# Kernel optimization log

Measured on AMD Instinct MI355X. Metric: run time of the kernel, lower is better.

The kernel has to match this reference:

```python
import jax, jax.numpy as jnp
import numpy as np

S = 512       # number of rnn_output rows (source positions)
T = 512       # number of target rows (queries)
DU = 512      # dim_u
DT = 512      # dim_target
D = DU + DT   # concat dim


def setup_inputs() -> dict:
    key = jax.random.key(0)
    k1, k2, k3, k4, k5, k6 = jax.random.split(key, 6)
    return {
        "rnn_outputs": jax.random.normal(k1, (S, DU), dtype=jnp.float32),
        "target": jax.random.normal(k2, (T, DT), dtype=jnp.float32),
        # nn.Linear(D, D): weight [D, D], bias [D]
        "W_lin": jax.random.normal(k3, (D, D), dtype=jnp.float32) * 0.02,
        "b_lin": jax.random.normal(k4, (D,), dtype=jnp.float32) * 0.02,
        # nn.Linear(D, 1): weight [1, D] stored flat, bias scalar
        "w_score": jax.random.normal(k5, (D,), dtype=jnp.float32) * 0.02,
        "b_score": jax.random.normal(k6, (), dtype=jnp.float32) * 0.02,
    }


def reference(rnn_outputs, target, W_lin, b_lin, w_score, b_score):
    du = rnn_outputs.shape[1]
    # linear(concat([rnn, tgt])) == rnn @ W[:, :du].T + tgt @ W[:, du:].T + b
    # (split the weight instead of materializing the [T, S, D] concat)
    A = rnn_outputs @ W_lin[:, :du].T            # [S, D]
    B = target @ W_lin[:, du:].T + b_lin         # [T, D]
    h = jnp.tanh(B[:, None, :] + A[None, :, :])  # [T, S, D]
    scores = h @ w_score + b_score               # [T, S]
    weights = jax.nn.softmax(scores, axis=1)     # softmax over source dim S
    # stack of per-row weighted sums == weights @ rnn_outputs
    return weights @ rnn_outputs                 # [T, dim_u]
```

## Files before the change

kernel.cpp:

```cpp
#include <hip/hip_runtime.h>


#define C2F 2.8853900817779268f

typedef __attribute__((ext_vector_type(8))) short short8;
typedef __attribute__((ext_vector_type(4))) float f32x4;
typedef __attribute__((ext_vector_type(2))) float f32x2;

__device__ __forceinline__ unsigned short bf16_rne(float f) {
    unsigned u = __builtin_bit_cast(unsigned, f);
    unsigned r = (u + 0x7FFFu + ((u >> 16) & 1u)) >> 16;
    return (unsigned short)r;
}
__device__ __forceinline__ float bf16_f(unsigned short h) {
    unsigned u = ((unsigned)h) << 16;
    return __builtin_bit_cast(float, u);
}
__device__ __forceinline__ f32x2 splat2(float s) {
    f32x2 r; r.x = s; r.y = s; return r;
}

__global__ __launch_bounds__(256, 4) void k1_mfma(
    const float* __restrict__ rnn, const float* __restrict__ tgt,
    const float* __restrict__ W, const float* __restrict__ bl,
    float* __restrict__ Abuf, float* __restrict__ Bbuf, int ksplit)
{
    __shared__ unsigned short Xh[64][40], Xl[64][40], Wh[64][40], Wl[64][40];
    const int j0 = blockIdx.x * 64;
    const int i0 = blockIdx.y * 64;
    const int kz = blockIdx.z;
    const int klen = 512 / ksplit;
    const int kbase = kz * klen;
    const bool isB = (i0 >= 512);
    const float* __restrict__ X = isB ? tgt : rnn;
    const int irow0 = isB ? (i0 - 512) : i0;
    const int koff = isB ? 512 : 0;
    const int tid = threadIdx.x;
    const int lane = tid & 63;
    const int wv = tid >> 6;
    const int isub = (wv & 1) * 32;
    const int jsub = (wv >> 1) * 32;
    const int srow = tid >> 2;
    const int skq  = tid & 3;
    const float* __restrict__ xp = X + (size_t)(irow0 + srow) * 512 + kbase + skq * 8;
    const float* __restrict__ wp = W + (size_t)(j0 + srow) * 1024 + koff + kbase + skq * 8;
    const int frow = lane & 15;
    const int fk   = (lane >> 4) * 8;
    f32x4 acc00 = {0.f,0.f,0.f,0.f}, acc01 = {0.f,0.f,0.f,0.f};
    f32x4 acc10 = {0.f,0.f,0.f,0.f}, acc11 = {0.f,0.f,0.f,0.f};
    float4 xv0 = *(const float4*)(xp);
    float4 xv1 = *(const float4*)(xp + 4);
    float4 wv0 = *(const float4*)(wp);
    float4 wv1 = *(const float4*)(wp + 4);
    for (int k0 = 0; k0 < klen; k0 += 32) {
        __syncthreads();
        {
            short8 xh8, xl8, wh8, wl8;
            const float xf[8] = {xv0.x, xv0.y, xv0.z, xv0.w, xv1.x, xv1.y, xv1.z, xv1.w};
            const float wf[8] = {wv0.x, wv0.y, wv0.z, wv0.w, wv1.x, wv1.y, wv1.z, wv1.w};
            #pragma unroll
            for (int e = 0; e < 8; ++e) {
                const unsigned short xh = bf16_rne(xf[e]);
                const unsigned short wh = bf16_rne(wf[e]);
                xh8[e] = (short)xh;
                wh8[e] = (short)wh;
                xl8[e] = (short)bf16_rne(xf[e] - bf16_f(xh));
                wl8[e] = (short)bf16_rne(wf[e] - bf16_f(wh));
            }
            *(short8*)&Xh[srow][skq * 8] = xh8;
            *(short8*)&Xl[srow][skq * 8] = xl8;
            *(short8*)&Wh[srow][skq * 8] = wh8;
            *(short8*)&Wl[srow][skq * 8] = wl8;
        }
        __syncthreads();
        if (k0 + 32 < klen) {
            xv0 = *(const float4*)(xp + k0 + 32);
            xv1 = *(const float4*)(xp + k0 + 36);
            wv0 = *(const float4*)(wp + k0 + 32);
            wv1 = *(const float4*)(wp + k0 + 36);
        }
        const short8 ah0 = *(const short8*)&Xh[isub + frow][fk];
        const short8 ah1 = *(const short8*)&Xh[isub + 16 + frow][fk];
        const short8 bh0 = *(const short8*)&Wh[jsub + frow][fk];
        const short8 bh1 = *(const short8*)&Wh[jsub + 16 + frow][fk];
        acc00 = __builtin_amdgcn_mfma_f32_16x16x32_bf16(ah0, bh0, acc00, 0, 0, 0);
        acc01 = __builtin_amdgcn_mfma_f32_16x16x32_bf16(ah0, bh1, acc01, 0, 0, 0);
        acc10 = __builtin_amdgcn_mfma_f32_16x16x32_bf16(ah1, bh0, acc10, 0, 0, 0);
        acc11 = __builtin_amdgcn_mfma_f32_16x16x32_bf16(ah1, bh1, acc11, 0, 0, 0);
        const short8 al0 = *(const short8*)&Xl[isub + frow][fk];
        const short8 al1 = *(const short8*)&Xl[isub + 16 + frow][fk];
        acc00 = __builtin_amdgcn_mfma_f32_16x16x32_bf16(al0, bh0, acc00, 0, 0, 0);
        acc01 = __builtin_amdgcn_mfma_f32_16x16x32_bf16(al0, bh1, acc01, 0, 0, 0);
        acc10 = __builtin_amdgcn_mfma_f32_16x16x32_bf16(al1, bh0, acc10, 0, 0, 0);
        acc11 = __builtin_amdgcn_mfma_f32_16x16x32_bf16(al1, bh1, acc11, 0, 0, 0);
        const short8 bl0 = *(const short8*)&Wl[jsub + frow][fk];
        const short8 bl1 = *(const short8*)&Wl[jsub + 16 + frow][fk];
        acc00 = __builtin_amdgcn_mfma_f32_16x16x32_bf16(ah0, bl0, acc00, 0, 0, 0);
        acc01 = __builtin_amdgcn_mfma_f32_16x16x32_bf16(ah0, bl1, acc01, 0, 0, 0);
        acc10 = __builtin_amdgcn_mfma_f32_16x16x32_bf16(ah1, bl0, acc10, 0, 0, 0);
        acc11 = __builtin_amdgcn_mfma_f32_16x16x32_bf16(ah1, bl1, acc11, 0, 0, 0);
    }
    const int orow = (lane >> 4) * 4;
    const int ocol = lane & 15;
    float* __restrict__ dst = (isB ? Bbuf : Abuf) + (size_t)kz * 524288;
    const bool addb = isB && (kz == ksplit - 1);
#define K1ST(ACC, MT, NT) do {                                            \
    const int jl = jsub + (NT)*16 + ocol;                                 \
    const float bb = addb ? bl[j0 + jl] : 0.f;                            \
    const int il = isub + (MT)*16 + orow;                                 \
    float4 o;                                                             \
    o.x = (ACC[0] + bb) * C2F;                                            \
    o.y = (ACC[1] + bb) * C2F;                                            \
    o.z = (ACC[2] + bb) * C2F;                                            \
    o.w = (ACC[3] + bb) * C2F;                                            \
    *(float4*)(dst + (size_t)(j0 + jl) * 512 + irow0 + il) = o;           \
} while (0)
    K1ST(acc00, 0, 0); K1ST(acc01, 0, 1); K1ST(acc10, 1, 0); K1ST(acc11, 1, 1);
#undef K1ST
}

#define K2P(ACC, PP, RR) do {                                                  \
    const f32x2 e0_ = __builtin_elementwise_fma(A0.PP, splat2(B0.RR), one2);   \
    const f32x2 e1_ = __builtin_elementwise_fma(A1.PP, splat2(B1.RR), one2);   \
    const f32x2 e2_ = __builtin_elementwise_fma(A2.PP, splat2(B2.RR), one2);   \
    const f32x2 e3_ = __builtin_elementwise_fma(A3.PP, splat2(B3.RR), one2);   \
    const f32x2 l01_ = e0_ * e1_;                                              \
    const f32x2 l23_ = e2_ * e3_;                                              \
    const f32x2 n01_ = __builtin_elementwise_fma(wx2, e1_, wy2 * e0_);         \
    const f32x2 n23_ = __builtin_elementwise_fma(wz2, e3_, ww2 * e2_);         \
    const f32x2 N_   = __builtin_elementwise_fma(n01_, l23_, n23_ * l01_);     \
    const f32x2 D_   = l01_ * l23_;                                            \
    f32x2 rd_;                                                                 \
    rd_.x = __builtin_amdgcn_rcpf(D_.x);                                       \
    rd_.y = __builtin_amdgcn_rcpf(D_.y);                                       \
    ACC = __builtin_elementwise_fma(N_, rd_, ACC);                             \
} while (0)

#define K2EXP(P0, P1) __builtin_amdgcn_exp2f(__builtin_fmaf(sumf, (P1), (P0)))

__global__ __launch_bounds__(256, 4) void k2_scores(
    const float* __restrict__ A0T, const float* __restrict__ A1T,
    const float* __restrict__ B0T, const float* __restrict__ B1T,
    const float* __restrict__ wsc, float* __restrict__ P, int dchunk, float sumf)
{
    __shared__ float at[32][68];
    __shared__ float bt[32][68];
    __shared__ float wl[128];
    const int s0 = blockIdx.x * 64;
    const int t0 = blockIdx.y * 64;
    const int dz = blockIdx.z * dchunk;
    const int tid = threadIdx.x;
    if (tid < dchunk) wl[tid] = wsc[dz + tid];
    const int drow = tid >> 3;
    const int sc8  = (tid & 7) * 8;
    const int ti   = tid >> 4;
    const int tj   = tid & 15;
    const float* __restrict__ Ar0 = A0T + (size_t)(dz + drow) * 512 + s0 + sc8;
    const float* __restrict__ Ar1 = A1T + (size_t)(dz + drow) * 512 + s0 + sc8;
    const float* __restrict__ Br0 = B0T + (size_t)(dz + drow) * 512 + t0 + sc8;
    const float* __restrict__ Br1 = B1T + (size_t)(dz + drow) * 512 + t0 + sc8;
    const f32x2 one2 = splat2(1.f);
    f32x2 ac0l = splat2(0.f), ac0h = splat2(0.f);
    f32x2 ac1l = splat2(0.f), ac1h = splat2(0.f);
    f32x2 ac2l = splat2(0.f), ac2h = splat2(0.f);
    f32x2 ac3l = splat2(0.f), ac3h = splat2(0.f);
    float4 pa00 = *(const float4*)(Ar0);
    float4 pa01 = *(const float4*)(Ar0 + 4);
    float4 pa10 = *(const float4*)(Ar1);
    float4 pa11 = *(const float4*)(Ar1 + 4);
    float4 pb00 = *(const float4*)(Br0);
    float4 pb01 = *(const float4*)(Br0 + 4);
    float4 pb10 = *(const float4*)(Br1);
    float4 pb11 = *(const float4*)(Br1 + 4);
    for (int c0 = 0; c0 < dchunk; c0 += 32) {
        __syncthreads();
        {
            float4 ea0, ea1, eb0, eb1;
            ea0.x = K2EXP(pa00.x, pa10.x);
            ea0.y = K2EXP(pa00.y, pa10.y);
            ea0.z = K2EXP(pa00.z, pa10.z);
            ea0.w = K2EXP(pa00.w, pa10.w);
            ea1.x = K2EXP(pa01.x, pa11.x);
            ea1.y = K2EXP(pa01.y, pa11.y);
            ea1.z = K2EXP(pa01.z, pa11.z);
            ea1.w = K2EXP(pa01.w, pa11.w);
            eb0.x = K2EXP(pb00.x, pb10.x);
            eb0.y = K2EXP(pb00.y, pb10.y);
            eb0.z = K2EXP(pb00.z, pb10.z);
            eb0.w = K2EXP(pb00.w, pb10.w);
            eb1.x = K2EXP(pb01.x, pb11.x);
            eb1.y = K2EXP(pb01.y, pb11.y);
            eb1.z = K2EXP(pb01.z, pb11.z);
            eb1.w = K2EXP(pb01.w, pb11.w);
            *(float4*)&at[drow][sc8]     = ea0;
            *(float4*)&at[drow][sc8 + 4] = ea1;
            *(float4*)&bt[drow][sc8]     = eb0;
            *(float4*)&bt[drow][sc8 + 4] = eb1;
        }
        __syncthreads();
        if (c0 + 32 < dchunk) {
            const size_t off = (size_t)(c0 + 32) * 512;
            pa00 = *(const float4*)(Ar0 + off);
            pa01 = *(const float4*)(Ar0 + off + 4);
            pa10 = *(const float4*)(Ar1 + off);
            pa11 = *(const float4*)(Ar1 + off + 4);
            pb00 = *(const float4*)(Br0 + off);
            pb01 = *(const float4*)(Br0 + off + 4);
            pb10 = *(const float4*)(Br1 + off);
            pb11 = *(const float4*)(Br1 + off + 4);
        }
        for (int dd = 0; dd < 32; dd += 4) {
            const float4 wa = *(const float4*)&wl[c0 + dd];
            const f32x2 wx2 = splat2(wa.x);
            const f32x2 wy2 = splat2(wa.y);
            const f32x2 wz2 = splat2(wa.z);
            const f32x2 ww2 = splat2(wa.w);
            const f32x4 A0 = *(const f32x4*)&at[dd + 0][tj * 4];
            const f32x4 A1 = *(const f32x4*)&at[dd + 1][tj * 4];
            const f32x4 A2 = *(const f32x4*)&at[dd + 2][tj * 4];
            const f32x4 A3 = *(const f32x4*)&at[dd + 3][tj * 4];
            const f32x4 B0 = *(const f32x4*)&bt[dd + 0][ti * 4];
            const f32x4 B1 = *(const f32x4*)&bt[dd + 1][ti * 4];
            const f32x4 B2 = *(const f32x4*)&bt[dd + 2][ti * 4];
            const f32x4 B3 = *(const f32x4*)&bt[dd + 3][ti * 4];
            K2P(ac0l, xy, x); K2P(ac0h, zw, x);
            K2P(ac1l, xy, y); K2P(ac1h, zw, y);
            K2P(ac2l, xy, z); K2P(ac2h, zw, z);
            K2P(ac3l, xy, w); K2P(ac3h, zw, w);
        }
    }
    float* __restrict__ Pz = P + (size_t)blockIdx.z * 512 * 512;
    float4 o0, o1, o2, o3;
    o0.x = ac0l.x; o0.y = ac0l.y; o0.z = ac0h.x; o0.w = ac0h.y;
    o1.x = ac1l.x; o1.y = ac1l.y; o1.z = ac1h.x; o1.w = ac1h.y;
    o2.x = ac2l.x; o2.y = ac2l.y; o2.z = ac2h.x; o2.w = ac2h.y;
    o3.x = ac3l.x; o3.y = ac3l.y; o3.z = ac3h.x; o3.w = ac3h.y;
    *(float4*)(Pz + (size_t)(t0 + ti * 4 + 0) * 512 + s0 + tj * 4) = o0;
    *(float4*)(Pz + (size_t)(t0 + ti * 4 + 1) * 512 + s0 + tj * 4) = o1;
    *(float4*)(Pz + (size_t)(t0 + ti * 4 + 2) * 512 + s0 + tj * 4) = o2;
    *(float4*)(Pz + (size_t)(t0 + ti * 4 + 3) * 512 + s0 + tj * 4) = o3;
}

__global__ __launch_bounds__(256, 4) void k3_softmax(
    const float* __restrict__ P, float* __restrict__ wgt, int nz)
{
    __shared__ float wm[4];
    __shared__ float wsum[4];
    const int t = blockIdx.x;
    const int tid = threadIdx.x;
    const size_t base = (size_t)t * 512 + tid * 2;
    float sx = 0.f, sy = 0.f;
    for (int z = 0; z < nz; ++z) {
        const float2 p = *(const float2*)(P + base + (size_t)z * 262144);
        sx += p.x; sy += p.y;
    }
    const float x0 = -2.f * sx;
    const float x1 = -2.f * sy;
    float m = fmaxf(x0, x1);
    #pragma unroll
    for (int off = 32; off; off >>= 1) m = fmaxf(m, __shfl_xor(m, off));
    if ((tid & 63) == 0) wm[tid >> 6] = m;
    __syncthreads();
    m = fmaxf(fmaxf(wm[0], wm[1]), fmaxf(wm[2], wm[3]));
    const float L2E = 1.4426950408889634f;
    const float e0 = __builtin_amdgcn_exp2f((x0 - m) * L2E);
    const float e1 = __builtin_amdgcn_exp2f((x1 - m) * L2E);
    float s = e0 + e1;
    #pragma unroll
    for (int off = 32; off; off >>= 1) s += __shfl_xor(s, off);
    if ((tid & 63) == 0) wsum[tid >> 6] = s;
    __syncthreads();
    s = wsum[0] + wsum[1] + wsum[2] + wsum[3];
    const float inv = 1.0f / s;
    float2 o; o.x = e0 * inv; o.y = e1 * inv;
    *(float2*)(wgt + (size_t)t * 512 + tid * 2) = o;
}

#define K4BFRAG(BH, BL, DCOL) do {                                      \
    _Pragma("unroll")                                                   \
    for (int e = 0; e < 8; ++e) {                                       \
        const float v_ = rs[fk + e][(DCOL)];                            \
        const unsigned short h_ = bf16_rne(v_);                         \
        (BH)[e] = (short)h_;                                            \
        (BL)[e] = (short)bf16_rne(v_ - bf16_f(h_));                     \
    }                                                                   \
} while (0)

__global__ __launch_bounds__(256, 4) void k4_mfma(
    const float* __restrict__ wgt, const float* __restrict__ rnn,
    float* __restrict__ P4)
{
    __shared__ unsigned short Gh[64][40], Gl[64][40];
    __shared__ float rs[32][69];
    const int d0g = blockIdx.x * 64;
    const int t0g = blockIdx.y * 64;
    const int z   = blockIdx.z;
    const int tid = threadIdx.x;
    const int lane = tid & 63;
    const int wv = tid >> 6;
    const int tsub = (wv & 1) * 32;
    const int dsub = (wv >> 1) * 32;
    const int trow = tid >> 2, skq = tid & 3;
    const int srw  = tid >> 3, cq  = tid & 7;
    const int frow = lane & 15;
    const int fk   = (lane >> 4) * 8;
    const int sbase = z * 64;
    f32x4 acc00 = {0.f,0.f,0.f,0.f}, acc01 = {0.f,0.f,0.f,0.f};
    f32x4 acc10 = {0.f,0.f,0.f,0.f}, acc11 = {0.f,0.f,0.f,0.f};
    const float* __restrict__ gp = wgt + (size_t)(t0g + trow) * 512 + sbase + skq * 8;
    const float* __restrict__ rp = rnn + (size_t)(sbase + srw) * 512 + d0g + cq * 8;
    float4 g0 = *(const float4*)(gp);
    float4 g1 = *(const float4*)(gp + 4);
    float4 r0 = *(const float4*)(rp);
    float4 r1 = *(const float4*)(rp + 4);
    #pragma unroll
    for (int c = 0; c < 2; ++c) {
        __syncthreads();
        {
            short8 gh8, gl8;
            const float gf[8] = {g0.x,g0.y,g0.z,g0.w,g1.x,g1.y,g1.z,g1.w};
            #pragma unroll
            for (int e = 0; e < 8; ++e) {
                const unsigned short h = bf16_rne(gf[e]);
                gh8[e] = (short)h;
                gl8[e] = (short)bf16_rne(gf[e] - bf16_f(h));
            }
            *(short8*)&Gh[trow][skq * 8] = gh8;
            *(short8*)&Gl[trow][skq * 8] = gl8;
            *(float4*)&rs[srw][cq * 8]     = r0;
            *(float4*)&rs[srw][cq * 8 + 4] = r1;
        }
        __syncthreads();
        if (c == 0) {
            g0 = *(const float4*)(gp + 32);
            g1 = *(const float4*)(gp + 36);
            r0 = *(const float4*)(rp + 32 * 512);
            r1 = *(const float4*)(rp + 32 * 512 + 4);
        }
        const short8 ah0 = *(const short8*)&Gh[tsub + frow][fk];
        const short8 ah1 = *(const short8*)&Gh[tsub + 16 + frow][fk];
        const short8 al0 = *(const short8*)&Gl[tsub + frow][fk];
        const short8 al1 = *(const short8*)&Gl[tsub + 16 + frow][fk];
        short8 bh0, bl0, bh1, bl1;
        K4BFRAG(bh0, bl0, dsub + frow);
        K4BFRAG(bh1, bl1, dsub + 16 + frow);
        acc00 = __builtin_amdgcn_mfma_f32_16x16x32_bf16(ah0, bh0, acc00, 0, 0, 0);
        acc01 = __builtin_amdgcn_mfma_f32_16x16x32_bf16(ah0, bh1, acc01, 0, 0, 0);
        acc10 = __builtin_amdgcn_mfma_f32_16x16x32_bf16(ah1, bh0, acc10, 0, 0, 0);
        acc11 = __builtin_amdgcn_mfma_f32_16x16x32_bf16(ah1, bh1, acc11, 0, 0, 0);
        acc00 = __builtin_amdgcn_mfma_f32_16x16x32_bf16(al0, bh0, acc00, 0, 0, 0);
        acc01 = __builtin_amdgcn_mfma_f32_16x16x32_bf16(al0, bh1, acc01, 0, 0, 0);
        acc10 = __builtin_amdgcn_mfma_f32_16x16x32_bf16(al1, bh0, acc10, 0, 0, 0);
        acc11 = __builtin_amdgcn_mfma_f32_16x16x32_bf16(al1, bh1, acc11, 0, 0, 0);
        acc00 = __builtin_amdgcn_mfma_f32_16x16x32_bf16(ah0, bl0, acc00, 0, 0, 0);
        acc01 = __builtin_amdgcn_mfma_f32_16x16x32_bf16(ah0, bl1, acc01, 0, 0, 0);
        acc10 = __builtin_amdgcn_mfma_f32_16x16x32_bf16(ah1, bl0, acc10, 0, 0, 0);
        acc11 = __builtin_amdgcn_mfma_f32_16x16x32_bf16(ah1, bl1, acc11, 0, 0, 0);
    }
    const int orow = (lane >> 4) * 4;
    const int ocol = lane & 15;
    float* __restrict__ Pz = P4 + (size_t)z * 262144;
#define K4ST(ACC, MT, NT) do {                                           \
    const int tl = tsub + (MT)*16 + orow;                                \
    const int dl = dsub + (NT)*16 + ocol;                                \
    float* p = Pz + (size_t)(t0g + tl) * 512 + d0g + dl;                 \
    p[0]    = ACC[0];                                                    \
    p[512]  = ACC[1];                                                    \
    p[1024] = ACC[2];                                                    \
    p[1536] = ACC[3];                                                    \
} while (0)
    K4ST(acc00, 0, 0); K4ST(acc01, 0, 1); K4ST(acc10, 1, 0); K4ST(acc11, 1, 1);
#undef K4ST
}

__global__ __launch_bounds__(256, 4) void k5_reduce(
    const float* __restrict__ P4, float* __restrict__ out)
{
    const int i = (blockIdx.x * 256 + threadIdx.x) * 4;
    float4 a = *(const float4*)(P4 + i);
    #pragma unroll
    for (int z = 1; z < 8; ++z) {
        const float4 b = *(const float4*)(P4 + (size_t)z * 262144 + i);
        a.x += b.x; a.y += b.y; a.z += b.z; a.w += b.w;
    }
    *(float4*)(out + i) = a;
}

extern "C" void kernel_launch(void* const* d_in, const int* in_sizes, int n_in,
                              void* d_out, int out_size, void* d_ws, size_t ws_size,
                              hipStream_t stream) {
    const float* rnn = (const float*)d_in[0];
    const float* tgt = (const float*)d_in[1];
    const float* W   = (const float*)d_in[2];
    const float* bl  = (const float*)d_in[3];
    const float* wsc = (const float*)d_in[4];
    float* out = (float*)d_out;

    const int nz = 8;
    const int dchunk = 1024 / nz;
    float* ws = (float*)d_ws;

    const bool split = (ws_size >= 17825792u);

    if (split) {
        float* A   = ws;
        float* B   = ws + 2 * 524288;
        float* P   = ws + 4 * 524288;
        float* wgt = P + (size_t)nz * 262144;
        float* P4  = P;
        k1_mfma   <<<dim3(16, 16, 2), 256, 0, stream>>>(rnn, tgt, W, bl, A, B, 2);
        k2_scores <<<dim3(8, 8, nz),  256, 0, stream>>>(A, A + 524288, B, B + 524288,
                                                        wsc, P, dchunk, 1.f);
        k3_softmax<<<512,             256, 0, stream>>>(P, wgt, nz);
        k4_mfma   <<<dim3(8, 8, 8),   256, 0, stream>>>(wgt, rnn, P4);
        k5_reduce <<<256,             256, 0, stream>>>(P4, out);
    } else {
        float* A   = ws;
        float* B   = ws + 524288;
        float* P   = ws + 2 * 524288;
        float* wgt = P + (size_t)nz * 262144;
        float* P4  = P;
        k1_mfma   <<<dim3(16, 16, 1), 256, 0, stream>>>(rnn, tgt, W, bl, A, B, 1);
        k2_scores <<<dim3(8, 8, nz),  256, 0, stream>>>(A, A, B, B, wsc, P, dchunk, 0.f);
        k3_softmax<<<512,             256, 0, stream>>>(P, wgt, nz);
        k4_mfma   <<<dim3(8, 8, 8),   256, 0, stream>>>(wgt, rnn, P4);
        k5_reduce <<<256,             256, 0, stream>>>(P4, out);
    }
}
```

Baseline: 55.74 us.

## Double-buffer LDS tiles in score kernel to overlap exp/stores with compute

Splits the score kernel's shared tiles into two ping-pong buffers. The exp transform and LDS write of the next d-chunk now happen while the current chunk is being computed, so one barrier per chunk is removed. The loop is hardcoded to 4 chunks of 32, which assumes dchunk equals 128 and ignores the runtime dchunk argument. It also doubles LDS use per block, which may limit occupancy.

```diff
diff --git a/kernel.cpp b/kernel.cpp
--- a/kernel.cpp
+++ b/kernel.cpp
@@ -120,10 +120,10 @@
 }
 
 #define K2P(ACC, PP, RR) do {                                                  \
-    const f32x2 e0_ = __builtin_elementwise_fma(A0.PP, splat2(B0.RR), one2);   \
-    const f32x2 e1_ = __builtin_elementwise_fma(A1.PP, splat2(B1.RR), one2);   \
-    const f32x2 e2_ = __builtin_elementwise_fma(A2.PP, splat2(B2.RR), one2);   \
-    const f32x2 e3_ = __builtin_elementwise_fma(A3.PP, splat2(B3.RR), one2);   \
+    const f32x2 e0_ = __builtin_elementwise_fma(A_0.PP, splat2(B_0.RR), one2); \
+    const f32x2 e1_ = __builtin_elementwise_fma(A_1.PP, splat2(B_1.RR), one2); \
+    const f32x2 e2_ = __builtin_elementwise_fma(A_2.PP, splat2(B_2.RR), one2); \
+    const f32x2 e3_ = __builtin_elementwise_fma(A_3.PP, splat2(B_3.RR), one2); \
     const f32x2 l01_ = e0_ * e1_;                                              \
     const f32x2 l23_ = e2_ * e3_;                                              \
     const f32x2 n01_ = __builtin_elementwise_fma(wx2, e1_, wy2 * e0_);         \
@@ -138,13 +138,71 @@
 
 #define K2EXP(P0, P1) __builtin_amdgcn_exp2f(__builtin_fmaf(sumf, (P1), (P0)))
 
+#define K2LOAD(CN) do {                                                        \
+    const size_t off_ = (size_t)(CN) * 32 * 512;                               \
+    pa00 = *(const float4*)(Ar0 + off_);                                       \
+    pa01 = *(const float4*)(Ar0 + off_ + 4);                                   \
+    pa10 = *(const float4*)(Ar1 + off_);                                       \
+    pa11 = *(const float4*)(Ar1 + off_ + 4);                                   \
+    pb00 = *(const float4*)(Br0 + off_);                                       \
+    pb01 = *(const float4*)(Br0 + off_ + 4);                                   \
+    pb10 = *(const float4*)(Br1 + off_);                                       \
+    pb11 = *(const float4*)(Br1 + off_ + 4);                                   \
+} while (0)
+
+#define K2WRITE(AT, BT) do {                                                   \
+    float4 ea0, ea1, eb0, eb1;                                                 \
+    ea0.x = K2EXP(pa00.x, pa10.x);                                             \
+    ea0.y = K2EXP(pa00.y, pa10.y);                                             \
+    ea0.z = K2EXP(pa00.z, pa10.z);                                             \
+    ea0.w = K2EXP(pa00.w, pa10.w);                                             \
+    ea1.x = K2EXP(pa01.x, pa11.x);                                             \
+    ea1.y = K2EXP(pa01.y, pa11.y);                                             \
+    ea1.z = K2EXP(pa01.z, pa11.z);                                             \
+    ea1.w = K2EXP(pa01.w, pa11.w);                                             \
+    eb0.x = K2EXP(pb00.x, pb10.x);                                             \
+    eb0.y = K2EXP(pb00.y, pb10.y);                                             \
+    eb0.z = K2EXP(pb00.z, pb10.z);                                             \
+    eb0.w = K2EXP(pb00.w, pb10.w);                                             \
+    eb1.x = K2EXP(pb01.x, pb11.x);                                             \
+    eb1.y = K2EXP(pb01.y, pb11.y);                                             \
+    eb1.z = K2EXP(pb01.z, pb11.z);                                             \
+    eb1.w = K2EXP(pb01.w, pb11.w);                                             \
+    *(float4*)&AT[drow][sc8]     = ea0;                                        \
+    *(float4*)&AT[drow][sc8 + 4] = ea1;                                        \
+    *(float4*)&BT[drow][sc8]     = eb0;                                        \
+    *(float4*)&BT[drow][sc8 + 4] = eb1;                                        \
+} while (0)
+
+#define K2COMP(AT, BT, WB) do {                                                \
+    for (int dd = 0; dd < 32; dd += 4) {                                       \
+        const float4 wa = *(const float4*)&wl[(WB) + dd];                      \
+        const f32x2 wx2 = splat2(wa.x);                                        \
+        const f32x2 wy2 = splat2(wa.y);                                        \
+        const f32x2 wz2 = splat2(wa.z);                                        \
+        const f32x2 ww2 = splat2(wa.w);                                        \
+        const f32x4 A_0 = *(const f32x4*)&AT[dd + 0][tj * 4];                  \
+        const f32x4 A_1 = *(const f32x4*)&AT[dd + 1][tj * 4];                  \
+        const f32x4 A_2 = *(const f32x4*)&AT[dd + 2][tj * 4];                  \
+        const f32x4 A_3 = *(const f32x4*)&AT[dd + 3][tj * 4];                  \
+        const f32x4 B_0 = *(const f32x4*)&BT[dd + 0][ti * 4];                  \
+        const f32x4 B_1 = *(const f32x4*)&BT[dd + 1][ti * 4];                  \
+        const f32x4 B_2 = *(const f32x4*)&BT[dd + 2][ti * 4];                  \
+        const f32x4 B_3 = *(const f32x4*)&BT[dd + 3][ti * 4];                  \
+        K2P(ac0l, xy, x); K2P(ac0h, zw, x);                                    \
+        K2P(ac1l, xy, y); K2P(ac1h, zw, y);                                    \
+        K2P(ac2l, xy, z); K2P(ac2h, zw, z);                                    \
+        K2P(ac3l, xy, w); K2P(ac3h, zw, w);                                    \
+    }                                                                          \
+} while (0)
+
 __global__ __launch_bounds__(256, 4) void k2_scores(
     const float* __restrict__ A0T, const float* __restrict__ A1T,
     const float* __restrict__ B0T, const float* __restrict__ B1T,
     const float* __restrict__ wsc, float* __restrict__ P, int dchunk, float sumf)
 {
-    __shared__ float at[32][68];
-    __shared__ float bt[32][68];
+    __shared__ float at0[32][68], bt0[32][68];
+    __shared__ float at1[32][68], bt1[32][68];
     __shared__ float wl[128];
     const int s0 = blockIdx.x * 64;
     const int t0 = blockIdx.y * 64;
@@ -164,69 +222,21 @@
     f32x2 ac1l = splat2(0.f), ac1h = splat2(0.f);
     f32x2 ac2l = splat2(0.f), ac2h = splat2(0.f);
     f32x2 ac3l = splat2(0.f), ac3h = splat2(0.f);
-    float4 pa00 = *(const float4*)(Ar0);
-    float4 pa01 = *(const float4*)(Ar0 + 4);
-    float4 pa10 = *(const float4*)(Ar1);
-    float4 pa11 = *(const float4*)(Ar1 + 4);
-    float4 pb00 = *(const float4*)(Br0);
-    float4 pb01 = *(const float4*)(Br0 + 4);
-    float4 pb10 = *(const float4*)(Br1);
-    float4 pb11 = *(const float4*)(Br1 + 4);
-    for (int c0 = 0; c0 < dchunk; c0 += 32) {
-        __syncthreads();
-        {
-            float4 ea0, ea1, eb0, eb1;
-            ea0.x = K2EXP(pa00.x, pa10.x);
-            ea0.y = K2EXP(pa00.y, pa10.y);
-            ea0.z = K2EXP(pa00.z, pa10.z);
-            ea0.w = K2EXP(pa00.w, pa10.w);
-            ea1.x = K2EXP(pa01.x, pa11.x);
-            ea1.y = K2EXP(pa01.y, pa11.y);
-            ea1.z = K2EXP(pa01.z, pa11.z);
-            ea1.w = K2EXP(pa01.w, pa11.w);
-            eb0.x = K2EXP(pb00.x, pb10.x);
-            eb0.y = K2EXP(pb00.y, pb10.y);
-            eb0.z = K2EXP(pb00.z, pb10.z);
-            eb0.w = K2EXP(pb00.w, pb10.w);
-            eb1.x = K2EXP(pb01.x, pb11.x);
-            eb1.y = K2EXP(pb01.y, pb11.y);
-            eb1.z = K2EXP(pb01.z, pb11.z);
-            eb1.w = K2EXP(pb01.w, pb11.w);
-            *(float4*)&at[drow][sc8]     = ea0;
-            *(float4*)&at[drow][sc8 + 4] = ea1;
-            *(float4*)&bt[drow][sc8]     = eb0;
-            *(float4*)&bt[drow][sc8 + 4] = eb1;
-        }
-        __syncthreads();
-        if (c0 + 32 < dchunk) {
-            const size_t off = (size_t)(c0 + 32) * 512;
-            pa00 = *(const float4*)(Ar0 + off);
-            pa01 = *(const float4*)(Ar0 + off + 4);
-            pa10 = *(const float4*)(Ar1 + off);
-            pa11 = *(const float4*)(Ar1 + off + 4);
-            pb00 = *(const float4*)(Br0 + off);
-            pb01 = *(const float4*)(Br0 + off + 4);
-            pb10 = *(const float4*)(Br1 + off);
-            pb11 = *(const float4*)(Br1 + off + 4);
-        }
-        for (int dd = 0; dd < 32; dd += 4) {
-            const float4 wa = *(const float4*)&wl[c0 + dd];
-            const f32x2 wx2 = splat2(wa.x);
-            const f32x2 wy2 = splat2(wa.y);
-            const f32x2 wz2 = splat2(wa.z);
-            const f32x2 ww2 = splat2(wa.w);
-            const f32x4 A0 = *(const f32x4*)&at[dd + 0][tj * 4];
-            const f32x4 A1 = *(const f32x4*)&at[dd + 1][tj * 4];
-            const f32x4 A2 = *(const f32x4*)&at[dd + 2][tj * 4];
-            const f32x4 A3 = *(const f32x4*)&at[dd + 3][tj * 4];
-            const f32x4 B0 = *(const f32x4*)&bt[dd + 0][ti * 4];
-            const f32x4 B1 = *(const f32x4*)&bt[dd + 1][ti * 4];
-            const f32x4 B2 = *(const f32x4*)&bt[dd + 2][ti * 4];
-            const f32x4 B3 = *(const f32x4*)&bt[dd + 3][ti * 4];
-            K2P(ac0l, xy, x); K2P(ac0h, zw, x);
-            K2P(ac1l, xy, y); K2P(ac1h, zw, y);
-            K2P(ac2l, xy, z); K2P(ac2h, zw, z);
-            K2P(ac3l, xy, w); K2P(ac3h, zw, w);
+    float4 pa00, pa01, pa10, pa11, pb00, pb01, pb10, pb11;
+    K2LOAD(0);
+    K2WRITE(at0, bt0);
+    for (int c0 = 0; c0 < 4; c0 += 2) {
+        __syncthreads();
+        K2LOAD(c0 + 1);
+        K2COMP(at0, bt0, c0 * 32);
+        K2WRITE(at1, bt1);
+        __syncthreads();
+        if (c0 + 2 < 4) {
+            K2LOAD(c0 + 2);
+            K2COMP(at1, bt1, c0 * 32 + 32);
+            K2WRITE(at0, bt0);
+        } else {
+            K2COMP(at1, bt1, c0 * 32 + 32);
         }
     }
     float* __restrict__ Pz = P + (size_t)blockIdx.z * 512 * 512;
```

Measured after the change: 55.96 us. Within noise of the previous version (+0.4%).
